# Kernel tuning notes

Hardware: AMD Instinct MI355X
Metric: run time of the kernel (lower is better)

The kernel has to match this reference:

```python
import jax, jax.numpy as jnp
import numpy as np

U = 356  # LSTM units

def _lstm(x, W, Wr, b, h0, c0):
    """Keras-style LSTM. x: [B,T,F]. Returns (hs [B,T,U], h [B,U], c [B,U])."""
    def step(carry, xt):
        h, c = carry
        z = xt @ W + h @ Wr + b            # [B, 4U], gate order i,f,g,o
        i, f, g, o = jnp.split(z, 4, axis=-1)
        c = jax.nn.sigmoid(f) * c + jax.nn.sigmoid(i) * jnp.tanh(g)
        h = jax.nn.sigmoid(o) * jnp.tanh(c)
        return (h, c), h
    (h, c), hs = jax.lax.scan(step, (h0, c0), jnp.swapaxes(x, 0, 1))
    return jnp.swapaxes(hs, 0, 1), h, c


def setup_inputs() -> dict:
    key = jax.random.key(0)
    ks = jax.random.split(key, 12)
    s = 0.05
    return {
        "x": jax.random.normal(ks[0], (8192, 7, 69), jnp.float32),
        "m": jax.random.normal(ks[1], (8192, 7, 45), jnp.float32),
        "enc_W": jax.random.normal(ks[2], (69, 4 * U), jnp.float32) * s,
        "enc_U": jax.random.normal(ks[3], (U, 4 * U), jnp.float32) * s,
        "enc_b": jnp.zeros((4 * U,), jnp.float32),
        "dec_W": jax.random.normal(ks[4], (45, 4 * U), jnp.float32) * s,
        "dec_U": jax.random.normal(ks[5], (U, 4 * U), jnp.float32) * s,
        "dec_b": jnp.zeros((4 * U,), jnp.float32),
        "W_map": jax.random.normal(ks[6], (7 * U, 1024), jnp.float32) * s,
        "b_map": jnp.zeros((1024,), jnp.float32),
        "W1": jax.random.normal(ks[7], (1024, 1024), jnp.float32) * s,
        "b1": jnp.zeros((1024,), jnp.float32),
        "W2": jax.random.normal(ks[8], (1024, 1024), jnp.float32) * s,
        "b2": jnp.zeros((1024,), jnp.float32),
        "W3": jax.random.normal(ks[9], (1024, 1024), jnp.float32) * s,
        "b3": jnp.zeros((1024,), jnp.float32),
        "W_out": jax.random.normal(ks[10], (1024, 168), jnp.float32) * s,
        "b_out": jnp.zeros((168,), jnp.float32),
    }


def reference(x, m, enc_W, enc_U, enc_b, dec_W, dec_U, dec_b,
              W_map, b_map, W1, b1, W2, b2, W3, b3, W_out, b_out):
    B = x.shape[0]
    h0 = jnp.zeros((B, U), x.dtype)
    c0 = jnp.zeros((B, U), x.dtype)
    # Encoder: only final states are used (dropout layers are identity at inference).
    _, s_h, s_c = _lstm(x, enc_W, enc_U, enc_b, h0, c0)
    # Decoder seeded with encoder states, returns full sequence [B,7,U].
    decoded, _, _ = _lstm(m, dec_W, dec_U, dec_b, s_h, s_c)
    f = decoded.reshape(B, -1)                     # [B, 7*356]
    h = jax.nn.relu(f @ W_map + b_map)
    h = jnp.tanh(h @ W1 + b1)
    h = jnp.tanh(h @ W2 + b2)
    h = jnp.tanh(h @ W3 + b3)
    return h @ W_out + b_out                        # [B, 168]
```

## Files before the change

### kernel.cpp

```cpp
#include <hip/hip_runtime.h>
#include <math.h>


using bf16x8 = __attribute__((ext_vector_type(8))) short;
using f32x4  = __attribute__((ext_vector_type(4))) float;

enum { EPI_NONE = 0, EPI_RELU = 1, EPI_TANH = 2 };

__device__ inline unsigned short f2bf(float f) {
    union { float f; unsigned u; } v; v.f = f;
    unsigned r = v.u + 0x7FFFu + ((v.u >> 16) & 1u);
    return (unsigned short)(r >> 16);
}
__device__ inline float sigf(float x) {
    return __fdividef(1.f, 1.f + __expf(-x));
}
__device__ inline float tanhfast(float x) {
    return 1.f - __fdividef(2.f, 1.f + __expf(2.f * x));
}

__device__ inline void gll16(const void* g, void* l) {
    __builtin_amdgcn_global_load_lds(
        (const __attribute__((address_space(1))) unsigned int*)(uintptr_t)g,
        (__attribute__((address_space(3))) unsigned int*)(unsigned int)(uintptr_t)l,
        16, 0, 0);
}

#define PROWS 32
#define PLDA  456

#define LOADB_G(dst, kkv, partv)                                               \
    _Pragma("unroll")                                                          \
    for (int q = 0; q < 4; ++q)                                                \
        dst[q] = *(const bf16x8*)(Wt + (size_t)(kkv) * 49152                   \
                                  + (w * 12 + (partv) * 4 + q) * 512           \
                                  + lane * 8);

#define LOADA(dst, kkv)                                                        \
    _Pragma("unroll")                                                          \
    for (int mi = 0; mi < 2; ++mi)                                             \
        dst[mi] = *(const bf16x8*)&Ab[(mi * 16 + lm) * PLDA + (kkv) * 32       \
                                      + quad * 8];

#define MFMA8(partv, bRv)                                                      \
    _Pragma("unroll")                                                          \
    for (int q = 0; q < 4; ++q) {                                              \
        acc[0][(partv) * 4 + q] = __builtin_amdgcn_mfma_f32_16x16x32_bf16(     \
            aF[0], bRv[q], acc[0][(partv) * 4 + q], 0, 0, 0);                  \
        acc[1][(partv) * 4 + q] = __builtin_amdgcn_mfma_f32_16x16x32_bf16(     \
            aF[1], bRv[q], acc[1][(partv) * 4 + q], 0, 0, 0);                  \
    }

#define VMWAIT(n)                                                              \
    asm volatile("s_waitcnt vmcnt(" #n ")" ::: "memory");                      \
    __builtin_amdgcn_sched_barrier(0);

__global__ __attribute__((amdgpu_flat_work_group_size(512, 512),
                          amdgpu_waves_per_eu(2, 2)))
void lstm_persist(const float* __restrict__ x,
                  const float* __restrict__ m,
                  const unsigned short* __restrict__ WtE,
                  const unsigned short* __restrict__ WtD,
                  const float* __restrict__ bIE,
                  const float* __restrict__ bID,
                  unsigned short* __restrict__ dcd)
{
    __shared__ __attribute__((aligned(16))) unsigned short Ab[PROWS * PLDA];
    const int tid  = threadIdx.x;
    const int lane = tid & 63;
    const int w    = tid >> 6;
    const int lm   = lane & 15, quad = lane >> 4;
    const int brow = blockIdx.x * PROWS;
    const int kk0  = blockIdx.x % 14;

    for (int i = tid; i < PROWS * PLDA; i += 512) Ab[i] = 0;
    __syncthreads();
    for (int i = tid; i < PROWS * 69; i += 512) {
        const int r = i / 69, f = i - r * 69;
        Ab[r * PLDA + f] = f2bf(x[((size_t)(brow + r) * 7 + 0) * 69 + f]);
    }

    float creg[2][3][4] = {};
    float bI[3][4];

    for (int s = 0; s < 14; ++s) {
        const bool enc = (s < 7);
        const int t = enc ? s : s - 7;
        const unsigned short* Wt = enc ? WtE : WtD;

        if (s == 0 || s == 7) {
            const float* bsrc = enc ? bIE : bID;
            #pragma unroll
            for (int a = 0; a < 3; ++a)
                #pragma unroll
                for (int g = 0; g < 4; ++g)
                    bI[a][g] = bsrc[(3 * w + a) * 64 + g * 16 + lm];
        }

        __syncthreads();

        f32x4 acc[2][12] = {};
        {
            bf16x8 b0[4], b1[4], b2[4];
            LOADB_G(b0, kk0, 0)
            LOADB_G(b1, kk0, 1)
            int kkc = kk0;
            #pragma unroll 1
            for (int i = 0; i < 14; ++i) {
                const int kkn = (kkc == 13) ? 0 : kkc + 1;
                bf16x8 aF[2];
                LOADB_G(b2, kkc, 2)
                VMWAIT(8)
                LOADA(aF, kkc)
                MFMA8(0, b0)
                if (i < 13) {
                    LOADB_G(b0, kkn, 0)
                    VMWAIT(8)
                } else {
                    VMWAIT(4)
                }
                MFMA8(1, b1)
                if (i < 13) {
                    LOADB_G(b1, kkn, 1)
                    VMWAIT(8)
                } else {
                    VMWAIT(0)
                }
                MFMA8(2, b2)
                kkc = kkn;
            }
        }

        __syncthreads();

        const int hoff = (s < 6) ? 69 : 45;
        #pragma unroll
        for (int mi = 0; mi < 2; ++mi)
            #pragma unroll
            for (int a = 0; a < 3; ++a) {
                const int u = (3 * w + a) * 16 + lm;
                const bool uok = (u < 356);
                #pragma unroll
                for (int r = 0; r < 4; ++r) {
                    const float zi = acc[mi][a * 4 + 0][r] + bI[a][0];
                    const float zf = acc[mi][a * 4 + 1][r] + bI[a][1];
                    const float zg = acc[mi][a * 4 + 2][r] + bI[a][2];
                    const float zo = acc[mi][a * 4 + 3][r] + bI[a][3];
                    const float cn = sigf(zf) * creg[mi][a][r]
                                   + sigf(zi) * tanhfast(zg);
                    creg[mi][a][r] = cn;
                    const unsigned short hb = f2bf(sigf(zo) * tanhfast(cn));
                    const int rl = mi * 16 + quad * 4 + r;
                    if (uok) {
                        if (s < 13) Ab[rl * PLDA + hoff + u] = hb;
                        if (!enc)
                            dcd[(size_t)(brow + rl) * 2496 + t * 356 + u] = hb;
                    }
                }
            }

        const int sn = s + 1;
        if (sn < 7) {
            for (int i = tid; i < PROWS * 69; i += 512) {
                const int r = i / 69, f = i - r * 69;
                Ab[r * PLDA + f] =
                    f2bf(x[((size_t)(brow + r) * 7 + sn) * 69 + f]);
            }
        } else if (sn < 14) {
            for (int i = tid; i < PROWS * 45; i += 512) {
                const int r = i / 45, f = i - r * 45;
                Ab[r * PLDA + f] =
                    f2bf(m[((size_t)(brow + r) * 7 + (sn - 7)) * 45 + f]);
            }
        }
    }
}


#define STAGE(A_, Bt_, K_, k0_, b_)                                            \
    {                                                                          \
        const int row = tid >> 2, kc = tid & 3;                                \
        gll16((A_)  + (size_t)(m0 + row) * (K_) + (k0_) + kc * 8,              \
              (void*)&As[b_][tid * 8]);                                        \
        gll16((Bt_) + (size_t)(n0 + row) * (K_) + (k0_) + kc * 8,              \
              (void*)&Bs[b_][tid * 8]);                                        \
    }

#define GEMM_CORE(A_, Bt_, K_)                                                 \
    STAGE(A_, Bt_, K_, 0, 0)                                                   \
    {                                                                          \
        const int niter = (K_) / 32;                                           \
        for (int it = 0; it < niter; ++it) {                                   \
            __syncthreads();                                                   \
            if (it + 1 < niter) {                                              \
                const int kn = (it + 1) * 32, bn = (it + 1) & 1;               \
                STAGE(A_, Bt_, K_, kn, bn)                                     \
            }                                                                  \
            const unsigned short* Asb = As[it & 1];                            \
            const unsigned short* Bsb = Bs[it & 1];                            \
            bf16x8 aF[2], bF[4];                                               \
            _Pragma("unroll")                                                  \
            for (int mi = 0; mi < 2; ++mi)                                     \
                aF[mi] = *(const bf16x8*)(Asb + (wr*32 + mi*16 + lm)*32 + quad*8);\
            _Pragma("unroll")                                                  \
            for (int ni = 0; ni < 4; ++ni)                                     \
                bF[ni] = *(const bf16x8*)(Bsb + (wc*64 + ni*16 + lm)*32 + quad*8);\
            _Pragma("unroll")                                                  \
            for (int mi = 0; mi < 2; ++mi)                                     \
                _Pragma("unroll")                                              \
                for (int ni = 0; ni < 4; ++ni)                                 \
                    acc[mi][ni] = __builtin_amdgcn_mfma_f32_16x16x32_bf16(     \
                        aF[mi], bF[ni], acc[mi][ni], 0, 0, 0);                 \
        }                                                                      \
    }

#define GEMM_PREAMBLE                                                          \
    __shared__ __attribute__((aligned(16))) unsigned short As[2][128 * 32];    \
    __shared__ __attribute__((aligned(16))) unsigned short Bs[2][128 * 32];    \
    const int tid  = threadIdx.x;                                              \
    const int lane = tid & 63;                                                 \
    const int w    = tid >> 6;                                       \
    const int wr   = w >> 1, wc = w & 1;                    \
    const int lm   = lane & 15, quad = lane >> 4;                              \
    const int m0   = blockIdx.x * 128, n0 = blockIdx.y * 128;                  \
    f32x4 acc[2][4] = {};

template <int EPI, int OUT_BF16, int NGUARD>
__global__ __launch_bounds__(512, 6)
void gemm_mfma(const unsigned short* __restrict__ A,
               const unsigned short* __restrict__ Bt,
               const float* __restrict__ bias,
               void* __restrict__ Cv, int ldc, int Nreal, int K)
{
    GEMM_PREAMBLE
    GEMM_CORE(A, Bt, K)
    #pragma unroll
    for (int mi = 0; mi < 2; ++mi)
        #pragma unroll
        for (int r = 0; r < 4; ++r) {
            const size_t row = m0 + wr * 32 + mi * 16 + quad * 4 + r;
            #pragma unroll
            for (int ni = 0; ni < 4; ++ni) {
                const int col = n0 + wc * 64 + ni * 16 + lm;
                if (!NGUARD || col < Nreal) {
                    float v = acc[mi][ni][r] + bias[col];
                    if (EPI == EPI_RELU) v = fmaxf(v, 0.f);
                    if (EPI == EPI_TANH) v = tanhfast(v);
                    if (OUT_BF16) ((unsigned short*)Cv)[row * ldc + col] = f2bf(v);
                    else          ((float*)Cv)[row * ldc + col] = v;
                }
            }
        }
}

struct PackArgs {
    const float *Wa0, *Wb0, *bias0; unsigned short* Wt0; float* bI0; int K10, K0, Kp0;
    const float *Wa1, *Wb1, *bias1; unsigned short* Wt1; float* bI1; int K11, K1, Kp1;
};
__global__ void pack_lstm2(PackArgs p)
{
    const float* Wa  = blockIdx.y ? p.Wa1  : p.Wa0;
    const float* Wb  = blockIdx.y ? p.Wb1  : p.Wb0;
    const float* bias= blockIdx.y ? p.bias1: p.bias0;
    unsigned short* Wt = blockIdx.y ? p.Wt1 : p.Wt0;
    float* biasI = blockIdx.y ? p.bI1 : p.bI0;
    const int K1 = blockIdx.y ? p.K11 : p.K10;
    const int K  = blockIdx.y ? p.K1  : p.K0;
    const int Kp = blockIdx.y ? p.Kp1 : p.Kp0;
    const int idx = blockIdx.x * 256 + threadIdx.x;
    if (idx >= 1536 * Kp) return;
    const int np = idx / Kp, k = idx - np * Kp;
    const int ub = np >> 6, g = (np >> 4) & 3, ul = np & 15;
    const int u = ub * 16 + ul;
    const bool valid = (u < 356);
    const int norig = g * 356 + u;
    float v = 0.f;
    if (valid && k < K)
        v = (k < K1) ? Wa[(size_t)k * 1424 + norig]
                     : Wb[(size_t)(k - K1) * 1424 + norig];
    const int wv = np / 192, rem = np - wv * 192;
    const int ni = rem >> 4, lmv = rem & 15;
    const int kkv = k >> 5, kq = k & 31;
    const int qd = kq >> 3, j = kq & 7;
    Wt[(size_t)kkv * 49152 + (size_t)(wv * 12 + ni) * 512 + (qd * 16 + lmv) * 8 + j]
        = f2bf(v);
    if (k == 0) biasI[np] = valid ? bias[norig] : 0.f;
}

__global__ void transpose_pack(const float* __restrict__ W, int K, int N,
                               unsigned short* __restrict__ Wt, int Kp, int Np)
{
    __shared__ float t[32][33];
    const int n0 = blockIdx.x * 32, k0 = blockIdx.y * 32;
    const int tx = threadIdx.x, ty = threadIdx.y;
    #pragma unroll
    for (int r = 0; r < 4; ++r) {
        const int k = k0 + ty + 8 * r, n = n0 + tx;
        t[ty + 8 * r][tx] = (k < K && n < N) ? W[(size_t)k * N + n] : 0.f;
    }
    __syncthreads();
    #pragma unroll
    for (int r = 0; r < 4; ++r) {
        const int k = k0 + tx, n = n0 + ty + 8 * r;
        if (k < Kp && n < Np) Wt[(size_t)n * Kp + k] = f2bf(t[tx][ty + 8 * r]);
    }
}

struct WP3 { const float *s0, *s1, *s2; unsigned short *d0, *d1, *d2; };
__global__ void transpose_pack3(WP3 p)
{
    __shared__ float t[32][33];
    const float* W = (blockIdx.z == 0) ? p.s0 : (blockIdx.z == 1) ? p.s1 : p.s2;
    unsigned short* Wt = (blockIdx.z == 0) ? p.d0 : (blockIdx.z == 1) ? p.d1 : p.d2;
    const int n0 = blockIdx.x * 32, k0 = blockIdx.y * 32;
    const int tx = threadIdx.x, ty = threadIdx.y;
    #pragma unroll
    for (int r = 0; r < 4; ++r)
        t[ty + 8 * r][tx] = W[(size_t)(k0 + ty + 8 * r) * 1024 + n0 + tx];
    __syncthreads();
    #pragma unroll
    for (int r = 0; r < 4; ++r)
        Wt[(size_t)(n0 + ty + 8 * r) * 1024 + k0 + tx] = f2bf(t[tx][ty + 8 * r]);
}

__global__ void zero_dcd_pad(unsigned short* __restrict__ dcd)
{
    const int i = blockIdx.x * 256 + threadIdx.x;
    if (i < 8192 * 4) dcd[(size_t)(i >> 2) * 2496 + 2492 + (i & 3)] = 0;
}

extern "C" void kernel_launch(void* const* d_in, const int* in_sizes, int n_in,
                              void* d_out, int out_size, void* d_ws, size_t ws_size,
                              hipStream_t stream)
{
    const float* x     = (const float*)d_in[0];
    const float* m     = (const float*)d_in[1];
    const float* enc_W = (const float*)d_in[2];
    const float* enc_U = (const float*)d_in[3];
    const float* enc_b = (const float*)d_in[4];
    const float* dec_W = (const float*)d_in[5];
    const float* dec_Um= (const float*)d_in[6];
    const float* dec_b = (const float*)d_in[7];
    const float* W_map = (const float*)d_in[8];
    const float* b_map = (const float*)d_in[9];
    const float* W1    = (const float*)d_in[10];
    const float* b1    = (const float*)d_in[11];
    const float* W2    = (const float*)d_in[12];
    const float* b2    = (const float*)d_in[13];
    const float* W3    = (const float*)d_in[14];
    const float* b3    = (const float*)d_in[15];
    const float* W_out = (const float*)d_in[16];
    const float* b_out = (const float*)d_in[17];
    float* out = (float*)d_out;

    const int B = 8192, FE = 69, FD = 45;
    const int KMP = 2496;

    char* ws = (char*)d_ws;
    size_t off = 0;
    auto alloc = [&](size_t bytes) -> void* {
        void* p = ws + off; off = (off + bytes + 255) & ~(size_t)255; return p;
    };
    unsigned short* WtE = (unsigned short*)alloc((size_t)1536 * 448 * 2);
    unsigned short* WtD = (unsigned short*)alloc((size_t)1536 * 448 * 2);
    unsigned short* WtM = (unsigned short*)alloc((size_t)1024 * KMP * 2);
    unsigned short* Wt1 = (unsigned short*)alloc((size_t)1024 * 1024 * 2);
    unsigned short* Wt2 = (unsigned short*)alloc((size_t)1024 * 1024 * 2);
    unsigned short* Wt3 = (unsigned short*)alloc((size_t)1024 * 1024 * 2);
    unsigned short* WtO = (unsigned short*)alloc((size_t)256 * 1024 * 2);
    float* bIE = (float*)alloc(1536 * 4);
    float* bID = (float*)alloc(1536 * 4);
    unsigned short* dcd = (unsigned short*)alloc((size_t)B * KMP * 2);
    unsigned short* a1  = (unsigned short*)alloc((size_t)B * 1024 * 2);
    unsigned short* a2  = (unsigned short*)alloc((size_t)B * 1024 * 2);

    PackArgs pa{enc_W, enc_U, enc_b, WtE, bIE, FE, FE + 356, 448,
                dec_W, dec_Um, dec_b, WtD, bID, FD, FD + 356, 448};
    pack_lstm2<<<dim3((1536 * 448 + 255) / 256, 2), 256, 0, stream>>>(pa);
    const dim3 tb(32, 8);
    transpose_pack<<<dim3(1024 / 32, KMP / 32), tb, 0, stream>>>(
        W_map, 2492, 1024, WtM, KMP, 1024);
    WP3 p3{W1, W2, W3, Wt1, Wt2, Wt3};
    transpose_pack3<<<dim3(32, 32, 3), tb, 0, stream>>>(p3);
    transpose_pack<<<dim3(256 / 32, 1024 / 32), tb, 0, stream>>>(
        W_out, 1024, 168, WtO, 1024, 256);
    zero_dcd_pad<<<(8192 * 4 + 255) / 256, 256, 0, stream>>>(dcd);

    lstm_persist<<<256, 512, 0, stream>>>(x, m, WtE, WtD, bIE, bID, dcd);

    gemm_mfma<EPI_RELU, 1, 0><<<dim3(64, 8), 512, 0, stream>>>(
        dcd, WtM, b_map, a1, 1024, 1024, KMP);
    gemm_mfma<EPI_TANH, 1, 0><<<dim3(64, 8), 512, 0, stream>>>(
        a1, Wt1, b1, a2, 1024, 1024, 1024);
    gemm_mfma<EPI_TANH, 1, 0><<<dim3(64, 8), 512, 0, stream>>>(
        a2, Wt2, b2, a1, 1024, 1024, 1024);
    gemm_mfma<EPI_TANH, 1, 0><<<dim3(64, 8), 512, 0, stream>>>(
        a1, Wt3, b3, a2, 1024, 1024, 1024);
    gemm_mfma<EPI_NONE, 0, 1><<<dim3(64, 2), 512, 0, stream>>>(
        a2, WtO, b_out, out, 168, 168, 1024);
}
```

Measured before the change: 565.8 us.

## Split LSTM gate columns across 12 waves instead of 8 in persistent kernel

The persistent LSTM kernel now launches 768 threads (12 waves) per block, each wave owning 2 unit tiles (8 gate column groups) instead of 3 (12). The K loop is restructured into a 3-way rotating register buffer for B fragments with two parts per k-step, unrolled by 3 with a tail. The intent is more waves per block to hide memory latency and fewer accumulator registers per wave, in exchange for a tighter per-wave register budget (waves_per_eu 3) and more per-block synchronization participants.

Result: slower. 692.6 us (+22.4%).

```diff
diff --git a/kernel.cpp b/kernel.cpp
--- a/kernel.cpp
+++ b/kernel.cpp
@@ -33,7 +33,7 @@
     _Pragma("unroll")                                                          \
     for (int q = 0; q < 4; ++q)                                                \
         dst[q] = *(const bf16x8*)(Wt + (size_t)(kkv) * 49152                   \
-                                  + (w * 12 + (partv) * 4 + q) * 512           \
+                                  + (w * 8 + (partv) * 4 + q) * 512            \
                                   + lane * 8);
 
 #define LOADA(dst, kkv)                                                        \
@@ -55,8 +55,8 @@
     asm volatile("s_waitcnt vmcnt(" #n ")" ::: "memory");                      \
     __builtin_amdgcn_sched_barrier(0);
 
-__global__ __attribute__((amdgpu_flat_work_group_size(512, 512),
-                          amdgpu_waves_per_eu(2, 2)))
+__global__ __attribute__((amdgpu_flat_work_group_size(768, 768),
+                          amdgpu_waves_per_eu(3, 3)))
 void lstm_persist(const float* __restrict__ x,
                   const float* __restrict__ m,
                   const unsigned short* __restrict__ WtE,
@@ -73,15 +73,15 @@
     const int brow = blockIdx.x * PROWS;
     const int kk0  = blockIdx.x % 14;
 
-    for (int i = tid; i < PROWS * PLDA; i += 512) Ab[i] = 0;
+    for (int i = tid; i < PROWS * PLDA; i += 768) Ab[i] = 0;
     __syncthreads();
-    for (int i = tid; i < PROWS * 69; i += 512) {
+    for (int i = tid; i < PROWS * 69; i += 768) {
         const int r = i / 69, f = i - r * 69;
         Ab[r * PLDA + f] = f2bf(x[((size_t)(brow + r) * 7 + 0) * 69 + f]);
     }
 
-    float creg[2][3][4] = {};
-    float bI[3][4];
+    float creg[2][2][4] = {};
+    float bI[2][4];
 
     for (int s = 0; s < 14; ++s) {
         const bool enc = (s < 7);
@@ -91,43 +91,64 @@
         if (s == 0 || s == 7) {
             const float* bsrc = enc ? bIE : bID;
             #pragma unroll
-            for (int a = 0; a < 3; ++a)
+            for (int uu = 0; uu < 2; ++uu)
                 #pragma unroll
                 for (int g = 0; g < 4; ++g)
-                    bI[a][g] = bsrc[(3 * w + a) * 64 + g * 16 + lm];
+                    bI[uu][g] = bsrc[(2 * w + uu) * 64 + g * 16 + lm];
         }
 
         __syncthreads();
 
-        f32x4 acc[2][12] = {};
+        f32x4 acc[2][8] = {};
         {
             bf16x8 b0[4], b1[4], b2[4];
             LOADB_G(b0, kk0, 0)
             LOADB_G(b1, kk0, 1)
-            int kkc = kk0;
+            int ka = kk0;
             #pragma unroll 1
-            for (int i = 0; i < 14; ++i) {
-                const int kkn = (kkc == 13) ? 0 : kkc + 1;
+            for (int it = 0; it < 4; ++it) {
+                const int kb = (ka == 13) ? 0 : ka + 1;
+                const int kc = (kb == 13) ? 0 : kb + 1;
+                const int kd = (kc == 13) ? 0 : kc + 1;
                 bf16x8 aF[2];
-                LOADB_G(b2, kkc, 2)
-                VMWAIT(8)
-                LOADA(aF, kkc)
+                LOADB_G(b2, kb, 0)
+                VMWAIT(8)
+                LOADA(aF, ka)
                 MFMA8(0, b0)
-                if (i < 13) {
-                    LOADB_G(b0, kkn, 0)
-                    VMWAIT(8)
-                } else {
-                    VMWAIT(4)
-                }
+                LOADB_G(b0, kb, 1)
+                VMWAIT(8)
                 MFMA8(1, b1)
-                if (i < 13) {
-                    LOADB_G(b1, kkn, 1)
-                    VMWAIT(8)
-                } else {
-                    VMWAIT(0)
-                }
-                MFMA8(2, b2)
-                kkc = kkn;
+                LOADB_G(b1, kc, 0)
+                VMWAIT(8)
+                LOADA(aF, kb)
+                MFMA8(0, b2)
+                LOADB_G(b2, kc, 1)
+                VMWAIT(8)
+                MFMA8(1, b0)
+                LOADB_G(b0, kd, 0)
+                VMWAIT(8)
+                LOADA(aF, kc)
+                MFMA8(0, b1)
+                LOADB_G(b1, kd, 1)
+                VMWAIT(8)
+                MFMA8(1, b2)
+                ka = kd;
+            }
+            {
+                const int kb = (ka == 13) ? 0 : ka + 1;
+                bf16x8 aF[2];
+                LOADB_G(b2, kb, 0)
+                VMWAIT(8)
+                LOADA(aF, ka)
+                MFMA8(0, b0)
+                LOADB_G(b0, kb, 1)
+                VMWAIT(8)
+                MFMA8(1, b1)
+                VMWAIT(4)
+                LOADA(aF, kb)
+                MFMA8(0, b2)
+                VMWAIT(0)
+                MFMA8(1, b0)
             }
         }
 
@@ -137,18 +158,18 @@
         #pragma unroll
         for (int mi = 0; mi < 2; ++mi)
             #pragma unroll
-            for (int a = 0; a < 3; ++a) {
-                const int u = (3 * w + a) * 16 + lm;
+            for (int uu = 0; uu < 2; ++uu) {
+                const int u = (2 * w + uu) * 16 + lm;
                 const bool uok = (u < 356);
                 #pragma unroll
                 for (int r = 0; r < 4; ++r) {
-                    const float zi = acc[mi][a * 4 + 0][r] + bI[a][0];
-                    const float zf = acc[mi][a * 4 + 1][r] + bI[a][1];
-                    const float zg = acc[mi][a * 4 + 2][r] + bI[a][2];
-                    const float zo = acc[mi][a * 4 + 3][r] + bI[a][3];
-                    const float cn = sigf(zf) * creg[mi][a][r]
+                    const float zi = acc[mi][uu * 4 + 0][r] + bI[uu][0];
+                    const float zf = acc[mi][uu * 4 + 1][r] + bI[uu][1];
+                    const float zg = acc[mi][uu * 4 + 2][r] + bI[uu][2];
+                    const float zo = acc[mi][uu * 4 + 3][r] + bI[uu][3];
+                    const float cn = sigf(zf) * creg[mi][uu][r]
                                    + sigf(zi) * tanhfast(zg);
-                    creg[mi][a][r] = cn;
+                    creg[mi][uu][r] = cn;
                     const unsigned short hb = f2bf(sigf(zo) * tanhfast(cn));
                     const int rl = mi * 16 + quad * 4 + r;
                     if (uok) {
@@ -161,13 +182,13 @@
 
         const int sn = s + 1;
         if (sn < 7) {
-            for (int i = tid; i < PROWS * 69; i += 512) {
+            for (int i = tid; i < PROWS * 69; i += 768) {
                 const int r = i / 69, f = i - r * 69;
                 Ab[r * PLDA + f] =
                     f2bf(x[((size_t)(brow + r) * 7 + sn) * 69 + f]);
             }
         } else if (sn < 14) {
-            for (int i = tid; i < PROWS * 45; i += 512) {
+            for (int i = tid; i < PROWS * 45; i += 768) {
                 const int r = i / 45, f = i - r * 45;
                 Ab[r * PLDA + f] =
                     f2bf(m[((size_t)(brow + r) * 7 + (sn - 7)) * 45 + f]);
@@ -386,7 +407,7 @@
         W_out, 1024, 168, WtO, 1024, 256);
     zero_dcd_pad<<<(8192 * 4 + 255) / 256, 256, 0, stream>>>(dcd);
 
-    lstm_persist<<<256, 512, 0, stream>>>(x, m, WtE, WtD, bIE, bID, dcd);
+    lstm_persist<<<256, 768, 0, stream>>>(x, m, WtE, WtD, bIE, bID, dcd);
 
     gemm_mfma<EPI_RELU, 1, 0><<<dim3(64, 8), 512, 0, stream>>>(
         dcd, WtM, b_map, a1, 1024, 1024, KMP);
```
